# Optimization experiments

Measured on AMD Instinct MI355X. Metric: run time of the kernel, lower is better.

The kernel has to match this reference:

```python
import jax, jax.numpy as jnp
import numpy as np

N_NODES = 20000
N_EDGES = 640000
D = 64        # node / edge feature dim
H = 128       # MLP hidden dim


def setup_inputs() -> dict:
    key = jax.random.key(0)
    ks = jax.random.split(key, 12)
    inp = {
        "x": jax.random.normal(ks[0], (N_NODES, D), dtype=jnp.float32),
        "edge_index": jax.random.randint(ks[1], (2, N_EDGES), 0, N_NODES, dtype=jnp.int64),
        "edge_attr": jax.random.normal(ks[2], (N_EDGES, D), dtype=jnp.float32),
        "f": jax.random.normal(ks[3], (N_NODES, D), dtype=jnp.float32),
        # edge MLP: concat(x_src, x_dest, edge_attr) = 3D -> H -> D
        "We1": jax.random.normal(ks[4], (3 * D, H), dtype=jnp.float32) / np.sqrt(3 * D),
        "be1": jnp.zeros((H,), dtype=jnp.float32),
        "We2": jax.random.normal(ks[5], (H, D), dtype=jnp.float32) / np.sqrt(H),
        "be2": jnp.zeros((D,), dtype=jnp.float32),
        # node MLP: concat(x, agg, f) = 3D -> H -> D
        "Wn1": jax.random.normal(ks[6], (3 * D, H), dtype=jnp.float32) / np.sqrt(3 * D),
        "bn1": jnp.zeros((H,), dtype=jnp.float32),
        "Wn2": jax.random.normal(ks[7], (H, D), dtype=jnp.float32) / np.sqrt(H),
        "bn2": jnp.zeros((D,), dtype=jnp.float32),
    }
    return inp


def reference(x, edge_index, edge_attr, f, We1, be1, We2, be2, Wn1, bn1, Wn2, bn2):
    src, dest = edge_index[0], edge_index[1]
    # edge model: MLP over gathered src/dest node features + edge attrs
    e_in = jnp.concatenate([x[src], x[dest], edge_attr], axis=-1)      # [E, 3D]
    e_h = jax.nn.relu(e_in @ We1 + be1)                                 # [E, H]
    edge_out = e_h @ We2 + be2                                          # [E, D]
    # node model: scatter-add edge messages to dest, then MLP
    agg = jax.ops.segment_sum(edge_out, dest, num_segments=N_NODES)    # [N, D]
    n_in = jnp.concatenate([x, agg, f], axis=-1)                        # [N, 3D]
    n_h = jax.nn.relu(n_in @ Wn1 + bn1)                                 # [N, H]
    x_out = n_h @ Wn2 + bn2                                             # [N, D]
    return (x_out, edge_out)
```

## Files before the change

kernel.cpp:

```cpp
#include <hip/hip_runtime.h>

#define NE 640000
#define NN 20000
#define SEI 200
#define SEH 136

typedef __attribute__((ext_vector_type(8))) short s16x8;
typedef __attribute__((ext_vector_type(4))) short s16x4;
typedef __attribute__((ext_vector_type(4))) float f32x4;

typedef const __attribute__((ext_vector_type(4))) float cf32x4;

__device__ __forceinline__ short f2bf(float f) {
  unsigned int u = __float_as_uint(f);
  u += 0x7fffu + ((u >> 16) & 1u);
  return (short)(u >> 16);
}

__device__ __forceinline__ s16x8 cvt8(f32x4 a, f32x4 b) {
  s16x8 o;
  o[0]=f2bf(a[0]); o[1]=f2bf(a[1]); o[2]=f2bf(a[2]); o[3]=f2bf(a[3]);
  o[4]=f2bf(b[0]); o[5]=f2bf(b[1]); o[6]=f2bf(b[2]); o[7]=f2bf(b[3]);
  return o;
}

__device__ __forceinline__ void load_wfrags_lds(const float* W1, const float* W2,
                                                const float* b1, const float* b2,
                                                short* smem, int t,
                                                int wv, int r, int g,
                                                s16x8 w1f[2][6], s16x8 w2f[4],
                                                f32x4 b1r[2], f32x4* b2r) {
  #pragma unroll
  for (int i = 0; i < 24; ++i) {
    int idx4 = t + i * 256;
    f32x4 v = ((cf32x4*)W1)[idx4];
    s16x4 pk; pk[0]=f2bf(v[0]); pk[1]=f2bf(v[1]); pk[2]=f2bf(v[2]); pk[3]=f2bf(v[3]);
    *(s16x4*)&smem[idx4 * 4] = pk;
  }
  __syncthreads();
  #pragma unroll
  for (int nn = 0; nn < 2; ++nn) {
    const int h = (wv*2+nn)*16 + r;
    #pragma unroll
    for (int kk = 0; kk < 6; ++kk) {
      s16x8 wf;
      #pragma unroll
      for (int i = 0; i < 8; ++i) wf[i] = smem[(kk*32 + g*8 + i)*128 + h];
      w1f[nn][kk] = wf;
    }
    b1r[nn] = *(cf32x4*)(b1 + (wv*2+nn)*16 + g*4);
  }
  __syncthreads();
  #pragma unroll
  for (int i = 0; i < 8; ++i) {
    int idx4 = t + i * 256;
    f32x4 v = ((cf32x4*)W2)[idx4];
    s16x4 pk; pk[0]=f2bf(v[0]); pk[1]=f2bf(v[1]); pk[2]=f2bf(v[2]); pk[3]=f2bf(v[3]);
    *(s16x4*)&smem[idx4 * 4] = pk;
  }
  __syncthreads();
  {
    const int h2 = wv*16 + r;
    #pragma unroll
    for (int kk = 0; kk < 4; ++kk) {
      s16x8 wf;
      #pragma unroll
      for (int i = 0; i < 8; ++i) wf[i] = smem[(kk*32 + g*8 + i)*64 + h2];
      w2f[kk] = wf;
    }
    *b2r = *(cf32x4*)(b2 + wv*16 + g*4);
  }
  __syncthreads();
}


__global__ void count_kernel(const int* __restrict__ eidx, int* __restrict__ cursor) {
  for (int e = blockIdx.x * blockDim.x + threadIdx.x; e < NE;
       e += gridDim.x * blockDim.x)
    atomicAdd(&cursor[eidx[NE + e]], 1);
}

__global__ __launch_bounds__(1024)
void scan_kernel(int* __restrict__ cursor, int* __restrict__ offs) {
  __shared__ int part[1024];
  const int t = threadIdx.x;
  const int CH = 20;
  const int lo = t * CH, hi = min(lo + CH, NN);
  int s = 0;
  for (int i = lo; i < hi; ++i) s += cursor[i];
  part[t] = s;
  __syncthreads();
  for (int d = 1; d < 1024; d <<= 1) {
    int u = (t >= d) ? part[t - d] : 0;
    __syncthreads();
    part[t] += u;
    __syncthreads();
  }
  int run = part[t] - s;
  for (int i = lo; i < hi; ++i) {
    int c = cursor[i];
    offs[i] = run;
    cursor[i] = run;
    run += c;
  }
  if (t == 1023) offs[NN] = NE;
}

__global__ void scatter_kernel(const int* __restrict__ eidx,
                               int* __restrict__ cursor, int* __restrict__ elist) {
  for (int e = blockIdx.x * blockDim.x + threadIdx.x; e < NE;
       e += gridDim.x * blockDim.x) {
    int pos = atomicAdd(&cursor[eidx[NE + e]], 1);
    elist[pos] = e;
  }
}

#define LOAD_ROWS(sv, dv, ee) do {                                        \
    cf32x4* ps_ = (cf32x4*)(x  + (size_t)(sv)*64 + p*16);                 \
    cf32x4* pd_ = (cf32x4*)(x  + (size_t)(dv)*64 + p*16);                 \
    cf32x4* pe_ = (cf32x4*)(ea + (size_t)(ee)*64 + p*16);                 \
    L[0]=ps_[0]; L[1]=ps_[1]; L[2]=ps_[2];  L[3]=ps_[3];                  \
    L[4]=pd_[0]; L[5]=pd_[1]; L[6]=pd_[2];  L[7]=pd_[3];                  \
    L[8]=pe_[0]; L[9]=pe_[1]; L[10]=pe_[2]; L[11]=pe_[3];                 \
  } while (0)

#define WRITE_EIN(buf) do {                                               \
    short* stg_ = (buf) + el*SEI + p*16;                                  \
    ((s16x8*)stg_)[0]       = cvt8(L[0], L[1]);                           \
    ((s16x8*)stg_)[1]       = cvt8(L[2], L[3]);                           \
    ((s16x8*)(stg_+64))[0]  = cvt8(L[4], L[5]);                           \
    ((s16x8*)(stg_+64))[1]  = cvt8(L[6], L[7]);                           \
    ((s16x8*)(stg_+128))[0] = cvt8(L[8], L[9]);                           \
    ((s16x8*)(stg_+128))[1] = cvt8(L[10], L[11]);                         \
  } while (0)

__global__ __launch_bounds__(256, 2)
void edge_kernel(const float* __restrict__ x, const int* __restrict__ eidx,
                 const float* __restrict__ ea,
                 const float* __restrict__ We1, const float* __restrict__ be1,
                 const float* __restrict__ We2, const float* __restrict__ be2,
                 float* __restrict__ edge_out)
{
  __shared__ __align__(16) char smem[68608];
  short* sEin0 = (short*)smem;
  short* sEin1 = (short*)(smem + 25600);
  short* sEh   = (short*)(smem + 51200);

  const int t = threadIdx.x;
  const int wv = t >> 6, lane = t & 63;
  const int r = lane & 15, g = lane >> 4;

  s16x8 w1f[2][6], w2f[4];
  f32x4 b1r[2], b2r;
  load_wfrags_lds(We1, We2, be1, be2, (short*)smem, t, wv, r, g,
                  w1f, w2f, b1r, &b2r);

  const int el = t >> 2, p = t & 3;
  const int nT = NE / 64;
  const int S = (int)gridDim.x;
  const f32x4 zero = {0.f, 0.f, 0.f, 0.f};

  f32x4 L[12];
  int sN = 0, dN = 0;
  int tile = blockIdx.x;

  if (tile < nT) {
    int e = (tile << 6) + el;
    int sv = eidx[e], dv = eidx[NE + e];
    LOAD_ROWS(sv, dv, e);
    WRITE_EIN(sEin0);
    const int t1 = tile + S;
    if (t1 < nT) {
      e = (t1 << 6) + el;
      sv = eidx[e]; dv = eidx[NE + e];
      LOAD_ROWS(sv, dv, e);
    }
    const int t2 = tile + 2 * S;
    if (t2 < nT) { e = (t2 << 6) + el; sN = eidx[e]; dN = eidx[NE + e]; }
  }
  __syncthreads();

  int cur = 0;
  while (tile < nT) {
    const short* Ecur = cur ? sEin1 : sEin0;
    short* Enxt = cur ? sEin0 : sEin1;
    const int tW = tile + S, tI = tile + 2 * S, tX = tile + 3 * S;
    if (tW < nT) WRITE_EIN(Enxt);
    if (tI < nT) { const int e = (tI << 6) + el; LOAD_ROWS(sN, dN, e); }
    if (tX < nT) { const int e = (tX << 6) + el; sN = eidx[e]; dN = eidx[NE + e]; }

    f32x4 acc1[2][4];
    #pragma unroll
    for (int nn = 0; nn < 2; ++nn)
      #pragma unroll
      for (int j = 0; j < 4; ++j) acc1[nn][j] = zero;
    #pragma unroll
    for (int kk = 0; kk < 6; ++kk) {
      #pragma unroll
      for (int j = 0; j < 4; ++j) {
        s16x8 ef = *(const s16x8*)&Ecur[(j*16 + r)*SEI + kk*32 + g*8];
        acc1[0][j] = __builtin_amdgcn_mfma_f32_16x16x32_bf16(w1f[0][kk], ef, acc1[0][j], 0, 0, 0);
        acc1[1][j] = __builtin_amdgcn_mfma_f32_16x16x32_bf16(w1f[1][kk], ef, acc1[1][j], 0, 0, 0);
      }
    }
    #pragma unroll
    for (int nn = 0; nn < 2; ++nn)
      #pragma unroll
      for (int j = 0; j < 4; ++j) {
        s16x4 pk;
        #pragma unroll
        for (int q = 0; q < 4; ++q) {
          float v = acc1[nn][j][q] + b1r[nn][q];
          pk[q] = f2bf(v > 0.f ? v : 0.f);
        }
        *(s16x4*)&sEh[(j*16 + r)*SEH + (wv*2+nn)*16 + g*4] = pk;
      }
    __syncthreads();

    const int ebase = tile << 6;
    #pragma unroll
    for (int j = 0; j < 4; ++j) {
      f32x4 a2 = zero;
      #pragma unroll
      for (int kk = 0; kk < 4; ++kk) {
        s16x8 hf = *(const s16x8*)&sEh[(j*16 + r)*SEH + kk*32 + g*8];
        a2 = __builtin_amdgcn_mfma_f32_16x16x32_bf16(w2f[kk], hf, a2, 0, 0, 0);
      }
      f32x4 v = a2 + b2r;
      *(f32x4*)&edge_out[(size_t)(ebase + j*16 + r)*64 + wv*16 + g*4] = v;
    }
    __syncthreads();
    cur ^= 1;
    tile += S;
  }
}

__global__ __launch_bounds__(256)
void agg_kernel(const float* __restrict__ eo, const int* __restrict__ offs,
                const int* __restrict__ elist, float* __restrict__ agg) {
  const int w = threadIdx.x >> 6;
  const int lane = threadIdx.x & 63;
  const int cg = lane & 15, rg = lane >> 4;
  for (int i = blockIdx.x * 4 + w; i < NN; i += (int)gridDim.x * 4) {
    const int end = offs[i + 1];
    f32x4 a0 = {0.f,0.f,0.f,0.f}, a1 = {0.f,0.f,0.f,0.f};
    int j = offs[i] + rg;
    for (; j + 4 < end; j += 8) {
      const int e0 = elist[j];
      const int e1 = elist[j + 4];
      a0 += *(cf32x4*)&eo[(size_t)e0*64 + cg*4];
      a1 += *(cf32x4*)&eo[(size_t)e1*64 + cg*4];
    }
    if (j < end) {
      const int e = elist[j];
      a0 += *(cf32x4*)&eo[(size_t)e*64 + cg*4];
    }
    f32x4 a = a0 + a1;
    #pragma unroll
    for (int q = 0; q < 4; ++q) {
      a[q] += __shfl_xor(a[q], 16);
      a[q] += __shfl_xor(a[q], 32);
    }
    if (rg == 0) *(f32x4*)&agg[(size_t)i*64 + cg*4] = a;
  }
}

__global__ __launch_bounds__(256, 2)
void node_kernel(const float* __restrict__ x, const float* agg,
                 const float* __restrict__ f,
                 const float* __restrict__ Wn1, const float* __restrict__ bn1,
                 const float* __restrict__ Wn2, const float* __restrict__ bn2,
                 float* x_out)
{
  __shared__ __align__(16) char smem[49152];
  short* sEin = (short*)smem;
  short* sEh  = (short*)(smem + 25600);

  const int t = threadIdx.x;
  const int wv = t >> 6, lane = t & 63;
  const int r = lane & 15, g = lane >> 4;

  s16x8 w1f[2][6], w2f[4];
  f32x4 b1r[2], b2r;
  load_wfrags_lds(Wn1, Wn2, bn1, bn2, (short*)smem, t, wv, r, g,
                  w1f, w2f, b1r, &b2r);

  const int el = t >> 2, p = t & 3;
  const f32x4 zero = {0.f, 0.f, 0.f, 0.f};
  const int base = blockIdx.x << 6;
  const int i = base + el;

  f32x4 L[12];
  if (i < NN) {
    cf32x4* ps_ = (cf32x4*)(x   + (size_t)i*64 + p*16);
    cf32x4* pa_ = (cf32x4*)(agg + (size_t)i*64 + p*16);
    cf32x4* pf_ = (cf32x4*)(f   + (size_t)i*64 + p*16);
    L[0]=ps_[0]; L[1]=ps_[1]; L[2]=ps_[2];  L[3]=ps_[3];
    L[4]=pa_[0]; L[5]=pa_[1]; L[6]=pa_[2];  L[7]=pa_[3];
    L[8]=pf_[0]; L[9]=pf_[1]; L[10]=pf_[2]; L[11]=pf_[3];
  } else {
    #pragma unroll
    for (int q = 0; q < 12; ++q) L[q] = zero;
  }
  WRITE_EIN(sEin);
  __syncthreads();

  f32x4 acc1[2][4];
  #pragma unroll
  for (int nn = 0; nn < 2; ++nn)
    #pragma unroll
    for (int j = 0; j < 4; ++j) acc1[nn][j] = zero;
  #pragma unroll
  for (int kk = 0; kk < 6; ++kk) {
    #pragma unroll
    for (int j = 0; j < 4; ++j) {
      s16x8 ef = *(const s16x8*)&sEin[(j*16 + r)*SEI + kk*32 + g*8];
      acc1[0][j] = __builtin_amdgcn_mfma_f32_16x16x32_bf16(w1f[0][kk], ef, acc1[0][j], 0, 0, 0);
      acc1[1][j] = __builtin_amdgcn_mfma_f32_16x16x32_bf16(w1f[1][kk], ef, acc1[1][j], 0, 0, 0);
    }
  }
  #pragma unroll
  for (int nn = 0; nn < 2; ++nn)
    #pragma unroll
    for (int j = 0; j < 4; ++j) {
      s16x4 pk;
      #pragma unroll
      for (int q = 0; q < 4; ++q) {
        float v = acc1[nn][j][q] + b1r[nn][q];
        pk[q] = f2bf(v > 0.f ? v : 0.f);
      }
      *(s16x4*)&sEh[(j*16 + r)*SEH + (wv*2+nn)*16 + g*4] = pk;
    }
  __syncthreads();

  #pragma unroll
  for (int j = 0; j < 4; ++j) {
    f32x4 a2 = zero;
    #pragma unroll
    for (int kk = 0; kk < 4; ++kk) {
      s16x8 hf = *(const s16x8*)&sEh[(j*16 + r)*SEH + kk*32 + g*8];
      a2 = __builtin_amdgcn_mfma_f32_16x16x32_bf16(w2f[kk], hf, a2, 0, 0, 0);
    }
    const int row = base + j*16 + r;
    if (row < NN) {
      f32x4 v = a2 + b2r;
      *(f32x4*)&x_out[(size_t)row*64 + wv*16 + g*4] = v;
    }
  }
}

extern "C" void kernel_launch(void* const* d_in, const int* in_sizes, int n_in,
                              void* d_out, int out_size, void* d_ws, size_t ws_size,
                              hipStream_t stream) {
  const float* x   = (const float*)d_in[0];
  const int*   ei  = (const int*)d_in[1];
  const float* ea  = (const float*)d_in[2];
  const float* f   = (const float*)d_in[3];
  const float* We1 = (const float*)d_in[4];
  const float* be1 = (const float*)d_in[5];
  const float* We2 = (const float*)d_in[6];
  const float* be2 = (const float*)d_in[7];
  const float* Wn1 = (const float*)d_in[8];
  const float* bn1 = (const float*)d_in[9];
  const float* Wn2 = (const float*)d_in[10];
  const float* bn2 = (const float*)d_in[11];

  float* x_out    = (float*)d_out;
  float* edge_out = x_out + (size_t)NN * 64;

  int* cursor = (int*)d_ws;
  int* offs   = cursor + NN;
  int* elist  = offs + NN + 8;

  hipMemsetAsync(cursor, 0, NN * sizeof(int), stream);
  count_kernel<<<1024, 256, 0, stream>>>(ei, cursor);
  scan_kernel<<<1, 1024, 0, stream>>>(cursor, offs);
  scatter_kernel<<<1024, 256, 0, stream>>>(ei, cursor, elist);
  edge_kernel<<<512, 256, 0, stream>>>(x, ei, ea, We1, be1, We2, be2, edge_out);
  agg_kernel<<<2048, 256, 0, stream>>>(edge_out, offs, elist, x_out);
  node_kernel<<<313, 256, 0, stream>>>(x, x_out, f, Wn1, bn1, Wn2, bn2, x_out);
}
```

Measured before the change: 252.6 us.

## Fuse scatter-add aggregation into edge kernel by processing edges in dest-sorted order

```diff
diff --git a/kernel.cpp b/kernel.cpp
--- a/kernel.cpp
+++ b/kernel.cpp
@@ -4,6 +4,7 @@
 #define NN 20000
 #define SEI 200
 #define SEH 136
+#define SEO 68
 
 typedef __attribute__((ext_vector_type(8))) short s16x8;
 typedef __attribute__((ext_vector_type(4))) short s16x4;
@@ -136,15 +137,20 @@
 
 __global__ __launch_bounds__(256, 2)
 void edge_kernel(const float* __restrict__ x, const int* __restrict__ eidx,
-                 const float* __restrict__ ea,
+                 const float* __restrict__ ea, const int* __restrict__ elist,
                  const float* __restrict__ We1, const float* __restrict__ be1,
                  const float* __restrict__ We2, const float* __restrict__ be2,
-                 float* __restrict__ edge_out)
+                 float* __restrict__ edge_out, float* __restrict__ agg)
 {
-  __shared__ __align__(16) char smem[68608];
+  __shared__ __align__(16) char smem[69632];
   short* sEin0 = (short*)smem;
   short* sEin1 = (short*)(smem + 25600);
   short* sEh   = (short*)(smem + 51200);
+  float* fEout = (float*)(smem + 51200);
+  int* sDest0  = (int*)(smem + 68608);
+  int* sDest1  = (int*)(smem + 68864);
+  int* sEid0   = (int*)(smem + 69120);
+  int* sEid1   = (int*)(smem + 69376);
 
   const int t = threadIdx.x;
   const int wv = t >> 6, lane = t & 63;
@@ -161,22 +167,27 @@
   const f32x4 zero = {0.f, 0.f, 0.f, 0.f};
 
   f32x4 L[12];
-  int sN = 0, dN = 0;
+  int eW = 0, dW = 0;
+  int eI = 0, sI = 0, dI = 0;
   int tile = blockIdx.x;
 
   if (tile < nT) {
-    int e = (tile << 6) + el;
-    int sv = eidx[e], dv = eidx[NE + e];
-    LOAD_ROWS(sv, dv, e);
+    int e0 = elist[(tile << 6) + el];
+    int s0 = eidx[e0], d0 = eidx[NE + e0];
+    LOAD_ROWS(s0, d0, e0);
     WRITE_EIN(sEin0);
+    if (p == 0) { sDest0[el] = d0; sEid0[el] = e0; }
     const int t1 = tile + S;
     if (t1 < nT) {
-      e = (t1 << 6) + el;
-      sv = eidx[e]; dv = eidx[NE + e];
-      LOAD_ROWS(sv, dv, e);
+      eW = elist[(t1 << 6) + el];
+      int sv = eidx[eW]; dW = eidx[NE + eW];
+      LOAD_ROWS(sv, dW, eW);
     }
     const int t2 = tile + 2 * S;
-    if (t2 < nT) { e = (t2 << 6) + el; sN = eidx[e]; dN = eidx[NE + e]; }
+    if (t2 < nT) {
+      eI = elist[(t2 << 6) + el];
+      sI = eidx[eI]; dI = eidx[NE + eI];
+    }
   }
   __syncthreads();
 
@@ -184,10 +195,21 @@
   while (tile < nT) {
     const short* Ecur = cur ? sEin1 : sEin0;
     short* Enxt = cur ? sEin0 : sEin1;
+    const int* sDestC = cur ? sDest1 : sDest0;
+    const int* sEidC  = cur ? sEid1  : sEid0;
+    int* sDestN = cur ? sDest0 : sDest1;
+    int* sEidN  = cur ? sEid0  : sEid1;
+
     const int tW = tile + S, tI = tile + 2 * S, tX = tile + 3 * S;
-    if (tW < nT) WRITE_EIN(Enxt);
-    if (tI < nT) { const int e = (tI << 6) + el; LOAD_ROWS(sN, dN, e); }
-    if (tX < nT) { const int e = (tX << 6) + el; sN = eidx[e]; dN = eidx[NE + e]; }
+    if (tW < nT) {
+      WRITE_EIN(Enxt);
+      if (p == 0) { sDestN[el] = dW; sEidN[el] = eW; }
+    }
+    if (tI < nT) { LOAD_ROWS(sI, dI, eI); eW = eI; dW = dI; }
+    if (tX < nT) {
+      eI = elist[(tX << 6) + el];
+      sI = eidx[eI]; dI = eidx[NE + eI];
+    }
 
     f32x4 acc1[2][4];
     #pragma unroll
@@ -217,7 +239,7 @@
       }
     __syncthreads();
 
-    const int ebase = tile << 6;
+    f32x4 a2s[4];
     #pragma unroll
     for (int j = 0; j < 4; ++j) {
       f32x4 a2 = zero;
@@ -226,42 +248,38 @@
         s16x8 hf = *(const s16x8*)&sEh[(j*16 + r)*SEH + kk*32 + g*8];
         a2 = __builtin_amdgcn_mfma_f32_16x16x32_bf16(w2f[kk], hf, a2, 0, 0, 0);
       }
-      f32x4 v = a2 + b2r;
-      *(f32x4*)&edge_out[(size_t)(ebase + j*16 + r)*64 + wv*16 + g*4] = v;
+      a2 += b2r;
+      a2s[j] = a2;
+      const int eg = sEidC[j*16 + r];
+      *(f32x4*)&edge_out[(size_t)eg*64 + wv*16 + g*4] = a2;
+    }
+    __syncthreads();
+
+    #pragma unroll
+    for (int j = 0; j < 4; ++j)
+      *(f32x4*)&fEout[(j*16 + r)*SEO + wv*16 + g*4] = a2s[j];
+    __syncthreads();
+
+    {
+      const int row0 = wv * 16;
+      float acc = fEout[row0*SEO + lane];
+      int dcur = sDestC[row0];
+      #pragma unroll
+      for (int k = 1; k < 16; ++k) {
+        const int dn = sDestC[row0 + k];
+        const float v = fEout[(row0 + k)*SEO + lane];
+        if (dn != dcur) {
+          unsafeAtomicAdd(&agg[(size_t)dcur*64 + lane], acc);
+          acc = v; dcur = dn;
+        } else {
+          acc += v;
+        }
+      }
+      unsafeAtomicAdd(&agg[(size_t)dcur*64 + lane], acc);
     }
     __syncthreads();
     cur ^= 1;
     tile += S;
-  }
-}
-
-__global__ __launch_bounds__(256)
-void agg_kernel(const float* __restrict__ eo, const int* __restrict__ offs,
-                const int* __restrict__ elist, float* __restrict__ agg) {
-  const int w = threadIdx.x >> 6;
-  const int lane = threadIdx.x & 63;
-  const int cg = lane & 15, rg = lane >> 4;
-  for (int i = blockIdx.x * 4 + w; i < NN; i += (int)gridDim.x * 4) {
-    const int end = offs[i + 1];
-    f32x4 a0 = {0.f,0.f,0.f,0.f}, a1 = {0.f,0.f,0.f,0.f};
-    int j = offs[i] + rg;
-    for (; j + 4 < end; j += 8) {
-      const int e0 = elist[j];
-      const int e1 = elist[j + 4];
-      a0 += *(cf32x4*)&eo[(size_t)e0*64 + cg*4];
-      a1 += *(cf32x4*)&eo[(size_t)e1*64 + cg*4];
-    }
-    if (j < end) {
-      const int e = elist[j];
-      a0 += *(cf32x4*)&eo[(size_t)e*64 + cg*4];
-    }
-    f32x4 a = a0 + a1;
-    #pragma unroll
-    for (int q = 0; q < 4; ++q) {
-      a[q] += __shfl_xor(a[q], 16);
-      a[q] += __shfl_xor(a[q], 32);
-    }
-    if (rg == 0) *(f32x4*)&agg[(size_t)i*64 + cg*4] = a;
   }
 }
 
@@ -372,11 +390,12 @@
   int* offs   = cursor + NN;
   int* elist  = offs + NN + 8;
 
+  hipMemsetAsync(x_out, 0, (size_t)NN * 64 * sizeof(float), stream);
   hipMemsetAsync(cursor, 0, NN * sizeof(int), stream);
   count_kernel<<<1024, 256, 0, stream>>>(ei, cursor);
   scan_kernel<<<1, 1024, 0, stream>>>(cursor, offs);
   scatter_kernel<<<1024, 256, 0, stream>>>(ei, cursor, elist);
-  edge_kernel<<<512, 256, 0, stream>>>(x, ei, ea, We1, be1, We2, be2, edge_out);
-  agg_kernel<<<2048, 256, 0, stream>>>(edge_out, offs, elist, x_out);
+  edge_kernel<<<512, 256, 0, stream>>>(x, ei, ea, elist, We1, be1, We2, be2,
+                                       edge_out, x_out);
   node_kernel<<<313, 256, 0, stream>>>(x, x_out, f, Wn1, bn1, Wn2, bn2, x_out);
 }
```

Measured after the change: 250.1 us. About the same (-1.0%).
